# Optimization experiments

Measured on AMD Instinct MI355X. Metric: run time of the kernel, lower is better.

Reference implementation:

```python
import jax, jax.numpy as jnp
import numpy as np

N = 100000          # active voxels
KS = 7              # kernel size per spatial dim
K = KS ** 3         # 343 kernel offsets
G = 64              # voxel grid extent
INPLANES = 128
PLANES = 128
D2 = PLANES // 4    # 32
EPS = 1e-5


def _build_neighbor_map(seed=0):
    # Random distinct voxel coordinates in a G^3 grid, then for every point and
    # every 7^3 offset find the index of the neighboring voxel (-1 if absent).
    rng = np.random.default_rng(seed)
    lin = rng.choice(G ** 3, size=N, replace=False)
    coords = np.stack(np.unravel_index(lin, (G, G, G)), axis=1).astype(np.int64)  # [N,3]
    keys = coords[:, 0] * G * G + coords[:, 1] * G + coords[:, 2]
    order = np.argsort(keys)
    skeys = keys[order]
    offs = np.arange(KS) - KS // 2
    off_grid = np.stack(np.meshgrid(offs, offs, offs, indexing='ij'), axis=-1).reshape(K, 3)
    q = coords[:, None, :] + off_grid[None, :, :]          # [N,K,3]
    inb = np.all((q >= 0) & (q < G), axis=-1)
    qk = q[..., 0] * G * G + q[..., 1] * G + q[..., 2]
    pos = np.searchsorted(skeys, qk)
    pos_c = np.clip(pos, 0, N - 1)
    found = inb & (skeys[pos_c] == qk)
    nbr = np.where(found, order[pos_c], -1).astype(np.int32)  # [N,K]
    return jnp.asarray(nbr)


def setup_inputs() -> dict:
    key = jax.random.key(0)
    k = jax.random.split(key, 4)
    feats = jax.random.normal(k[0], (N, INPLANES), jnp.float32)
    w1 = jax.random.normal(k[1], (INPLANES, D2), jnp.float32) / np.sqrt(INPLANES)
    w_conv = jax.random.normal(k[2], (K, D2, D2), jnp.float32) / np.sqrt(K * D2)
    w2 = jax.random.normal(k[3], (D2, PLANES), jnp.float32) / np.sqrt(D2)
    return {
        'feats': feats,
        'nbr': _build_neighbor_map(),
        'w1': w1,
        'ln1_g': jnp.ones((D2,), jnp.float32),
        'ln1_b': jnp.zeros((D2,), jnp.float32),
        'w_conv': w_conv,
        'w2': w2,
        'ln2_g': jnp.ones((PLANES,), jnp.float32),
        'ln2_b': jnp.zeros((PLANES,), jnp.float32),
    }


def _layernorm(x, g, b):
    m = jnp.mean(x, axis=-1, keepdims=True)
    v = jnp.var(x, axis=-1, keepdims=True)
    return (x - m) * jax.lax.rsqrt(v + EPS) * g + b


def _sparse_conv(x, nbr, w):
    # x: [N,d2], nbr: [N,K], w: [K,d2,d2]; gather-apply-scatter per kernel offset.
    def step(acc, inp):
        idx, wk = inp                                # idx: [N], wk: [d2,d2]
        valid = (idx >= 0).astype(x.dtype)[:, None]
        g = jnp.take(x, jnp.maximum(idx, 0), axis=0) * valid
        return acc + g @ wk, None
    acc0 = jnp.zeros((x.shape[0], w.shape[2]), x.dtype)
    out, _ = jax.lax.scan(step, acc0, (nbr.T, w))
    return out


def reference(feats, nbr, w1, ln1_g, ln1_b, w_conv, w2, ln2_g, ln2_b):
    shortcut = feats                                  # inplanes == planes -> Identity
    h = _layernorm(feats @ w1, ln1_g, ln1_b)          # unary_1: [N,d2]
    h = _sparse_conv(h, nbr, w_conv)                  # 7^3 sparse conv: [N,d2]
    h = _layernorm(h @ w2, ln2_g, ln2_b)              # unary_2: [N,planes]
    h = jax.nn.gelu(h, approximate=False)             # drop_path is Identity (rate 0)
    return h + shortcut
```

## Files before the change

kernel.cpp:

```cpp
#include <hip/hip_runtime.h>
#include <hip/hip_bf16.h>

#define N_PTS 100000
#define KOFF 343
#define EPS 1e-5f
#define NTILES 3125
#define SSTR 173

typedef __hip_bfloat16 bf16;
typedef __attribute__((ext_vector_type(4))) float f32x4;
typedef __attribute__((ext_vector_type(16))) float f32x16;
typedef __attribute__((ext_vector_type(8))) short s16x8;

__global__ __launch_bounds__(256) void pack_kernel(const float* __restrict__ w_conv,
                                                   bf16* __restrict__ wpk) {
  int t = blockIdx.x * 256 + threadIdx.x;
  if (t >= KOFF * 128) return;
  int l = t & 63;
  int s = (t >> 6) & 1;
  int k = t >> 7;
  int col = l & 31;
  int kq = l >> 5;
  const float* wk = w_conv + k * 1024;
  s16x8 v;
  for (int j = 0; j < 8; ++j) {
    bf16 h = __float2bfloat16(wk[(s * 16 + kq * 8 + j) * 32 + col]);
    short sv;
    __builtin_memcpy(&sv, &h, 2);
    v[j] = sv;
  }
  *reinterpret_cast<s16x8*>(reinterpret_cast<char*>(wpk) + (size_t)t * 16) = v;
}

__global__ __launch_bounds__(256) void unary1_kernel(const float* __restrict__ feats,
    const float* __restrict__ w1, const float* __restrict__ g1,
    const float* __restrict__ b1, bf16* __restrict__ h1b) {
  __shared__ float sf[8][128];
  __shared__ float sw[128 * 32];
  int tid = threadIdx.x;
  int rbase = blockIdx.x * 8;
  for (int i = tid; i < 1024; i += 256)
    reinterpret_cast<f32x4*>(sw)[i] = reinterpret_cast<const f32x4*>(w1)[i];
  {
    int i = tid;
    int r = rbase + (i >> 5);
    f32x4 v = reinterpret_cast<const f32x4*>(feats)[(size_t)r * 32 + (i & 31)];
    reinterpret_cast<f32x4*>(&sf[0][0])[i] = v;
  }
  __syncthreads();
  int half = tid >> 5;
  int c = tid & 31;
  int r = rbase + half;
  const float* frow = sf[half];
  float acc = 0.f;
  #pragma unroll 8
  for (int kk = 0; kk < 128; ++kk)
    acc += frow[kk] * sw[kk * 32 + c];
  float s = acc, s2 = acc * acc;
  #pragma unroll
  for (int m = 16; m >= 1; m >>= 1) {
    s  += __shfl_xor(s,  m, 64);
    s2 += __shfl_xor(s2, m, 64);
  }
  float mean = s * (1.f / 32.f);
  float var  = s2 * (1.f / 32.f) - mean * mean;
  float y = (acc - mean) * rsqrtf(var + EPS) * g1[c] + b1[c];
  h1b[(size_t)r * 32 + c] = __float2bfloat16(y);
}

template<int KCNT, int KBASE>
__device__ __forceinline__ void process_round(const int* __restrict__ snbr,
    const bf16* __restrict__ h1b, const s16x8* __restrict__ wb,
    f32x16& acc, int wave, int l, int col, int kq) {
  int k0 = (KCNT * wave) >> 2;
  int k1 = (KCNT * (wave + 1)) >> 2;
  const int* myrow = snbr + col * SSTR;
  const s16x8 zv = {0, 0, 0, 0, 0, 0, 0, 0};
  for (int kb = k0; kb < k1; kb += 4) {
    int id[4];
    s16x8 A0[4], A1[4], B0[4], B1[4];
    #pragma unroll
    for (int j = 0; j < 4; ++j) {
      int k = kb + j;
      id[j] = (k < k1) ? myrow[k] : -1;
    }
    #pragma unroll
    for (int j = 0; j < 4; ++j) {
      int k = kb + j;
      int kc = (k < k1) ? k : (k1 - 1);
      const s16x8* r = reinterpret_cast<const s16x8*>(h1b + (size_t)(id[j] < 0 ? 0 : id[j]) * 32);
      A0[j] = r[kq];
      A1[j] = r[2 + kq];
      B0[j] = wb[(size_t)(KBASE + kc) * 128 + l];
      B1[j] = wb[(size_t)(KBASE + kc) * 128 + 64 + l];
    }
    #pragma unroll
    for (int j = 0; j < 4; ++j) {
      s16x8 a0 = id[j] < 0 ? zv : A0[j];
      s16x8 a1 = id[j] < 0 ? zv : A1[j];
      acc = __builtin_amdgcn_mfma_f32_32x32x16_bf16(a0, B0[j], acc, 0, 0, 0);
      acc = __builtin_amdgcn_mfma_f32_32x32x16_bf16(a1, B1[j], acc, 0, 0, 0);
    }
  }
}

__global__ __launch_bounds__(256) void conv_r2_kernel(const bf16* __restrict__ h1b,
    const int* __restrict__ nbr, const bf16* __restrict__ wpk,
    float* __restrict__ h2) {
  __shared__ int sbuf[32 * SSTR];
  int tid = threadIdx.x;
  int wave = tid >> 6;
  int l = tid & 63;
  int col = l & 31;
  int kq = l >> 5;
  int pbase = blockIdx.x * 32;
  const int* g = nbr + (size_t)pbase * KOFF;
  const s16x8* wb = reinterpret_cast<const s16x8*>(wpk);
  f32x16 acc;
  #pragma unroll
  for (int i = 0; i < 16; ++i) acc[i] = 0.f;

  for (int i = tid; i < 32 * 172; i += 256) {
    int row = i / 172;
    int kk = i - row * 172;
    sbuf[row * SSTR + kk] = g[row * KOFF + kk];
  }
  __syncthreads();
  process_round<172, 0>(sbuf, h1b, wb, acc, wave, l, col, kq);
  __syncthreads();
  for (int i = tid; i < 32 * 171; i += 256) {
    int row = i / 171;
    int kk = i - row * 171;
    sbuf[row * SSTR + kk] = g[row * KOFF + 172 + kk];
  }
  __syncthreads();
  process_round<171, 172>(sbuf, h1b, wb, acc, wave, l, col, kq);
  __syncthreads();

  float* red = reinterpret_cast<float*>(sbuf);
  #pragma unroll
  for (int reg = 0; reg < 16; ++reg) {
    int rrow = (reg & 3) + 8 * (reg >> 2) + 4 * kq;
    red[wave * 1024 + rrow * 32 + col] = acc[reg];
  }
  __syncthreads();
  const f32x4* rv = reinterpret_cast<const f32x4*>(red);
  f32x4 s = rv[tid] + rv[256 + tid] + rv[512 + tid] + rv[768 + tid];
  reinterpret_cast<f32x4*>(h2 + (size_t)pbase * 32)[tid] = s;
}

__global__ __launch_bounds__(256) void unary2_kernel(const float* __restrict__ h2,
    const float* __restrict__ w2, const float* __restrict__ g2,
    const float* __restrict__ b2, const float* __restrict__ feats,
    float* __restrict__ out) {
  int tid = threadIdx.x;
  int wave = tid >> 6;
  int l = tid & 63;
  int r0 = blockIdx.x * 8 + wave * 2;
  const f32x4* h0 = reinterpret_cast<const f32x4*>(h2 + (size_t)r0 * 32);
  const f32x4* h1r = reinterpret_cast<const f32x4*>(h2 + (size_t)(r0 + 1) * 32);
  float a00 = 0.f, a01 = 0.f, a10 = 0.f, a11 = 0.f;
  #pragma unroll
  for (int q = 0; q < 8; ++q) {
    f32x4 v0 = h0[q];
    f32x4 v1 = h1r[q];
    #pragma unroll
    for (int j = 0; j < 4; ++j) {
      int kk = q * 4 + j;
      float wlo = w2[kk * 128 + l];
      float whi = w2[kk * 128 + 64 + l];
      a00 += v0[j] * wlo;  a01 += v0[j] * whi;
      a10 += v1[j] * wlo;  a11 += v1[j] * whi;
    }
  }
  float s0 = a00 + a01, q0 = a00 * a00 + a01 * a01;
  float s1 = a10 + a11, q1 = a10 * a10 + a11 * a11;
  #pragma unroll
  for (int m = 32; m >= 1; m >>= 1) {
    s0 += __shfl_xor(s0, m, 64);
    q0 += __shfl_xor(q0, m, 64);
    s1 += __shfl_xor(s1, m, 64);
    q1 += __shfl_xor(q1, m, 64);
  }
  float m0 = s0 * (1.f / 128.f);
  float v0 = q0 * (1.f / 128.f) - m0 * m0;
  float i0 = rsqrtf(v0 + EPS);
  float m1 = s1 * (1.f / 128.f);
  float v1 = q1 * (1.f / 128.f) - m1 * m1;
  float i1 = rsqrtf(v1 + EPS);
  float glo = g2[l], ghi = g2[64 + l];
  float blo = b2[l], bhi = b2[64 + l];
  float y00 = (a00 - m0) * i0 * glo + blo;
  float y01 = (a01 - m0) * i0 * ghi + bhi;
  float y10 = (a10 - m1) * i1 * glo + blo;
  float y11 = (a11 - m1) * i1 * ghi + bhi;
  float e00 = 0.5f * y00 * (1.f + erff(y00 * 0.70710678118f));
  float e01 = 0.5f * y01 * (1.f + erff(y01 * 0.70710678118f));
  float e10 = 0.5f * y10 * (1.f + erff(y10 * 0.70710678118f));
  float e11 = 0.5f * y11 * (1.f + erff(y11 * 0.70710678118f));
  out[(size_t)r0 * 128 + l]            = e00 + feats[(size_t)r0 * 128 + l];
  out[(size_t)r0 * 128 + 64 + l]       = e01 + feats[(size_t)r0 * 128 + 64 + l];
  out[(size_t)(r0 + 1) * 128 + l]      = e10 + feats[(size_t)(r0 + 1) * 128 + l];
  out[(size_t)(r0 + 1) * 128 + 64 + l] = e11 + feats[(size_t)(r0 + 1) * 128 + 64 + l];
}

extern "C" void kernel_launch(void* const* d_in, const int* in_sizes, int n_in,
                              void* d_out, int out_size, void* d_ws, size_t ws_size,
                              hipStream_t stream) {
  const float* feats  = (const float*)d_in[0];
  const int*   nbr    = (const int*)d_in[1];
  const float* w1     = (const float*)d_in[2];
  const float* ln1_g  = (const float*)d_in[3];
  const float* ln1_b  = (const float*)d_in[4];
  const float* w_conv = (const float*)d_in[5];
  const float* w2     = (const float*)d_in[6];
  const float* ln2_g  = (const float*)d_in[7];
  const float* ln2_b  = (const float*)d_in[8];
  float* out = (float*)d_out;
  char* ws = (char*)d_ws;
  bf16*  h1b = (bf16*)ws;
  bf16*  wpk = (bf16*)(ws + 6400000);
  float* h2  = (float*)(ws + 7102464);

  hipLaunchKernelGGL(pack_kernel,    dim3((KOFF * 128 + 255) / 256), dim3(256), 0, stream, w_conv, wpk);
  hipLaunchKernelGGL(unary1_kernel,  dim3(N_PTS / 8),                dim3(256), 0, stream, feats, w1, ln1_g, ln1_b, h1b);
  hipLaunchKernelGGL(conv_r2_kernel, dim3(NTILES),                   dim3(256), 0, stream, h1b, nbr, wpk, h2);
  hipLaunchKernelGGL(unary2_kernel,  dim3(N_PTS / 8),                dim3(256), 0, stream, h2, w2, ln2_g, ln2_b, feats, out);
}
```

Measured before the change: 309.4 us.

## Switch sparse conv MFMA from 32x32x16 to four 16x16x32 tiles

Replaces the single 32x32x16 bf16 MFMA accumulator per wave with four 16x16x32 MFMAs covering two 16-point row groups and two 16-channel column halves. The packed weight layout and the gather pattern change to match, so each lane now loads a full 16-byte chunk of a neighbor row for two points. The aim is better gather coalescing, since more lanes share the same neighbor row, and use of the smaller MFMA shape. In exchange each wave issues twice as many MFMA instructions and more index loads from shared memory.

Result: slower. 316.0 us (+2.1%).

```diff
diff --git a/kernel.cpp b/kernel.cpp
--- a/kernel.cpp
+++ b/kernel.cpp
@@ -9,7 +9,6 @@
 
 typedef __hip_bfloat16 bf16;
 typedef __attribute__((ext_vector_type(4))) float f32x4;
-typedef __attribute__((ext_vector_type(16))) float f32x16;
 typedef __attribute__((ext_vector_type(8))) short s16x8;
 
 __global__ __launch_bounds__(256) void pack_kernel(const float* __restrict__ w_conv,
@@ -17,14 +16,14 @@
   int t = blockIdx.x * 256 + threadIdx.x;
   if (t >= KOFF * 128) return;
   int l = t & 63;
-  int s = (t >> 6) & 1;
+  int cn = (t >> 6) & 1;
   int k = t >> 7;
-  int col = l & 31;
-  int kq = l >> 5;
+  int rr = l & 15;
+  int q = l >> 4;
   const float* wk = w_conv + k * 1024;
   s16x8 v;
   for (int j = 0; j < 8; ++j) {
-    bf16 h = __float2bfloat16(wk[(s * 16 + kq * 8 + j) * 32 + col]);
+    bf16 h = __float2bfloat16(wk[(q * 8 + j) * 32 + cn * 16 + rr]);
     short sv;
     __builtin_memcpy(&sv, &h, 2);
     v[j] = sv;
@@ -71,54 +70,57 @@
 template<int KCNT, int KBASE>
 __device__ __forceinline__ void process_round(const int* __restrict__ snbr,
     const bf16* __restrict__ h1b, const s16x8* __restrict__ wb,
-    f32x16& acc, int wave, int l, int col, int kq) {
+    f32x4& acc00, f32x4& acc01, f32x4& acc10, f32x4& acc11, int wave, int l) {
   int k0 = (KCNT * wave) >> 2;
   int k1 = (KCNT * (wave + 1)) >> 2;
-  const int* myrow = snbr + col * SSTR;
+  int rr = l & 15;
+  int q = l >> 4;
+  const int* row0 = snbr + rr * SSTR;
+  const int* row1 = snbr + (16 + rr) * SSTR;
+  const s16x8* h1s8 = reinterpret_cast<const s16x8*>(h1b);
   const s16x8 zv = {0, 0, 0, 0, 0, 0, 0, 0};
   for (int kb = k0; kb < k1; kb += 4) {
-    int id[4];
+    int id0[4], id1[4];
     s16x8 A0[4], A1[4], B0[4], B1[4];
     #pragma unroll
     for (int j = 0; j < 4; ++j) {
       int k = kb + j;
-      id[j] = (k < k1) ? myrow[k] : -1;
+      id0[j] = (k < k1) ? row0[k] : -1;
+      id1[j] = (k < k1) ? row1[k] : -1;
     }
     #pragma unroll
     for (int j = 0; j < 4; ++j) {
       int k = kb + j;
       int kc = (k < k1) ? k : (k1 - 1);
-      const s16x8* r = reinterpret_cast<const s16x8*>(h1b + (size_t)(id[j] < 0 ? 0 : id[j]) * 32);
-      A0[j] = r[kq];
-      A1[j] = r[2 + kq];
+      A0[j] = h1s8[(size_t)(id0[j] < 0 ? 0 : id0[j]) * 4 + q];
+      A1[j] = h1s8[(size_t)(id1[j] < 0 ? 0 : id1[j]) * 4 + q];
       B0[j] = wb[(size_t)(KBASE + kc) * 128 + l];
       B1[j] = wb[(size_t)(KBASE + kc) * 128 + 64 + l];
     }
     #pragma unroll
     for (int j = 0; j < 4; ++j) {
-      s16x8 a0 = id[j] < 0 ? zv : A0[j];
-      s16x8 a1 = id[j] < 0 ? zv : A1[j];
-      acc = __builtin_amdgcn_mfma_f32_32x32x16_bf16(a0, B0[j], acc, 0, 0, 0);
-      acc = __builtin_amdgcn_mfma_f32_32x32x16_bf16(a1, B1[j], acc, 0, 0, 0);
-    }
-  }
-}
-
-__global__ __launch_bounds__(256) void conv_r2_kernel(const bf16* __restrict__ h1b,
+      s16x8 a0 = id0[j] < 0 ? zv : A0[j];
+      s16x8 a1 = id1[j] < 0 ? zv : A1[j];
+      acc00 = __builtin_amdgcn_mfma_f32_16x16x32_bf16(a0, B0[j], acc00, 0, 0, 0);
+      acc01 = __builtin_amdgcn_mfma_f32_16x16x32_bf16(a0, B1[j], acc01, 0, 0, 0);
+      acc10 = __builtin_amdgcn_mfma_f32_16x16x32_bf16(a1, B0[j], acc10, 0, 0, 0);
+      acc11 = __builtin_amdgcn_mfma_f32_16x16x32_bf16(a1, B1[j], acc11, 0, 0, 0);
+    }
+  }
+}
+
+__global__ __launch_bounds__(256) void conv16_kernel(const bf16* __restrict__ h1b,
     const int* __restrict__ nbr, const bf16* __restrict__ wpk,
     float* __restrict__ h2) {
   __shared__ int sbuf[32 * SSTR];
   int tid = threadIdx.x;
   int wave = tid >> 6;
   int l = tid & 63;
-  int col = l & 31;
-  int kq = l >> 5;
   int pbase = blockIdx.x * 32;
   const int* g = nbr + (size_t)pbase * KOFF;
   const s16x8* wb = reinterpret_cast<const s16x8*>(wpk);
-  f32x16 acc;
-  #pragma unroll
-  for (int i = 0; i < 16; ++i) acc[i] = 0.f;
+  f32x4 acc00 = {0.f, 0.f, 0.f, 0.f}, acc01 = {0.f, 0.f, 0.f, 0.f};
+  f32x4 acc10 = {0.f, 0.f, 0.f, 0.f}, acc11 = {0.f, 0.f, 0.f, 0.f};
 
   for (int i = tid; i < 32 * 172; i += 256) {
     int row = i / 172;
@@ -126,7 +128,7 @@
     sbuf[row * SSTR + kk] = g[row * KOFF + kk];
   }
   __syncthreads();
-  process_round<172, 0>(sbuf, h1b, wb, acc, wave, l, col, kq);
+  process_round<172, 0>(sbuf, h1b, wb, acc00, acc01, acc10, acc11, wave, l);
   __syncthreads();
   for (int i = tid; i < 32 * 171; i += 256) {
     int row = i / 171;
@@ -134,14 +136,19 @@
     sbuf[row * SSTR + kk] = g[row * KOFF + 172 + kk];
   }
   __syncthreads();
-  process_round<171, 172>(sbuf, h1b, wb, acc, wave, l, col, kq);
+  process_round<171, 172>(sbuf, h1b, wb, acc00, acc01, acc10, acc11, wave, l);
   __syncthreads();
 
   float* red = reinterpret_cast<float*>(sbuf);
-  #pragma unroll
-  for (int reg = 0; reg < 16; ++reg) {
-    int rrow = (reg & 3) + 8 * (reg >> 2) + 4 * kq;
-    red[wave * 1024 + rrow * 32 + col] = acc[reg];
+  int rr = l & 15;
+  int q = l >> 4;
+  #pragma unroll
+  for (int reg = 0; reg < 4; ++reg) {
+    int prow = q * 4 + reg;
+    red[wave * 1024 + prow * 32 + rr]             = acc00[reg];
+    red[wave * 1024 + prow * 32 + 16 + rr]        = acc01[reg];
+    red[wave * 1024 + (16 + prow) * 32 + rr]      = acc10[reg];
+    red[wave * 1024 + (16 + prow) * 32 + 16 + rr] = acc11[reg];
   }
   __syncthreads();
   const f32x4* rv = reinterpret_cast<const f32x4*>(red);
@@ -224,6 +231,6 @@
 
   hipLaunchKernelGGL(pack_kernel,    dim3((KOFF * 128 + 255) / 256), dim3(256), 0, stream, w_conv, wpk);
   hipLaunchKernelGGL(unary1_kernel,  dim3(N_PTS / 8),                dim3(256), 0, stream, feats, w1, ln1_g, ln1_b, h1b);
-  hipLaunchKernelGGL(conv_r2_kernel, dim3(NTILES),                   dim3(256), 0, stream, h1b, nbr, wpk, h2);
+  hipLaunchKernelGGL(conv16_kernel,  dim3(NTILES),                   dim3(256), 0, stream, h1b, nbr, wpk, h2);
   hipLaunchKernelGGL(unary2_kernel,  dim3(N_PTS / 8),                dim3(256), 0, stream, h2, w2, ln2_g, ln2_b, feats, out);
 }
```

## Restructure sparse conv so each wave owns 32 points and weights stage through LDS

Applied to the files above, without the earlier changes.

The conv kernel no longer splits the 343 offsets across four waves with a cross-wave LDS reduction. Each block now handles 128 points, one 32-point tile per wave, and walks all offsets in chunks of 16. Each chunk's neighbor indices and packed bf16 weights are staged into shared memory and reused by all four waves. Missing neighbors are redirected to an appended zero row of h1b, which removes the per-element select, and the weights are zero-padded to 352 offsets. The aim is to cut global weight traffic and the final reduction, at the cost of more barriers per block and fewer blocks (782 instead of 3125) for hiding gather latency.

Result: slower. 453.5 us (+46.6%).

```diff
diff --git a/kernel.cpp b/kernel.cpp
--- a/kernel.cpp
+++ b/kernel.cpp
@@ -3,9 +3,11 @@
 
 #define N_PTS 100000
 #define KOFF 343
+#define KPAD 352
+#define KC 16
+#define NCH 22
 #define EPS 1e-5f
-#define NTILES 3125
-#define SSTR 173
+#define SIDX_STR 17
 
 typedef __hip_bfloat16 bf16;
 typedef __attribute__((ext_vector_type(4))) float f32x4;
@@ -13,23 +15,25 @@
 typedef __attribute__((ext_vector_type(8))) short s16x8;
 
 __global__ __launch_bounds__(256) void pack_kernel(const float* __restrict__ w_conv,
-                                                   bf16* __restrict__ wpk) {
+                                                   bf16* __restrict__ wpk2) {
   int t = blockIdx.x * 256 + threadIdx.x;
-  if (t >= KOFF * 128) return;
+  if (t >= KPAD * 128) return;
   int l = t & 63;
   int s = (t >> 6) & 1;
   int k = t >> 7;
   int col = l & 31;
   int kq = l >> 5;
-  const float* wk = w_conv + k * 1024;
-  s16x8 v;
-  for (int j = 0; j < 8; ++j) {
-    bf16 h = __float2bfloat16(wk[(s * 16 + kq * 8 + j) * 32 + col]);
-    short sv;
-    __builtin_memcpy(&sv, &h, 2);
-    v[j] = sv;
-  }
-  *reinterpret_cast<s16x8*>(reinterpret_cast<char*>(wpk) + (size_t)t * 16) = v;
+  s16x8 v = {0, 0, 0, 0, 0, 0, 0, 0};
+  if (k < KOFF) {
+    const float* wk = w_conv + k * 1024;
+    for (int j = 0; j < 8; ++j) {
+      bf16 h = __float2bfloat16(wk[(s * 16 + kq * 8 + j) * 32 + col]);
+      short sv;
+      __builtin_memcpy(&sv, &h, 2);
+      v[j] = sv;
+    }
+  }
+  *reinterpret_cast<s16x8*>(reinterpret_cast<char*>(wpk2) + (size_t)t * 16) = v;
 }
 
 __global__ __launch_bounds__(256) void unary1_kernel(const float* __restrict__ feats,
@@ -39,6 +43,8 @@
   __shared__ float sw[128 * 32];
   int tid = threadIdx.x;
   int rbase = blockIdx.x * 8;
+  if (blockIdx.x == 0 && tid < 16)
+    reinterpret_cast<int*>(h1b)[N_PTS * 16 + tid] = 0;
   for (int i = tid; i < 1024; i += 256)
     reinterpret_cast<f32x4*>(sw)[i] = reinterpret_cast<const f32x4*>(w1)[i];
   {
@@ -68,85 +74,73 @@
   h1b[(size_t)r * 32 + c] = __float2bfloat16(y);
 }
 
-template<int KCNT, int KBASE>
-__device__ __forceinline__ void process_round(const int* __restrict__ snbr,
-    const bf16* __restrict__ h1b, const s16x8* __restrict__ wb,
-    f32x16& acc, int wave, int l, int col, int kq) {
-  int k0 = (KCNT * wave) >> 2;
-  int k1 = (KCNT * (wave + 1)) >> 2;
-  const int* myrow = snbr + col * SSTR;
-  const s16x8 zv = {0, 0, 0, 0, 0, 0, 0, 0};
-  for (int kb = k0; kb < k1; kb += 4) {
-    int id[4];
-    s16x8 A0[4], A1[4], B0[4], B1[4];
-    #pragma unroll
-    for (int j = 0; j < 4; ++j) {
-      int k = kb + j;
-      id[j] = (k < k1) ? myrow[k] : -1;
-    }
-    #pragma unroll
-    for (int j = 0; j < 4; ++j) {
-      int k = kb + j;
-      int kc = (k < k1) ? k : (k1 - 1);
-      const s16x8* r = reinterpret_cast<const s16x8*>(h1b + (size_t)(id[j] < 0 ? 0 : id[j]) * 32);
-      A0[j] = r[kq];
-      A1[j] = r[2 + kq];
-      B0[j] = wb[(size_t)(KBASE + kc) * 128 + l];
-      B1[j] = wb[(size_t)(KBASE + kc) * 128 + 64 + l];
-    }
-    #pragma unroll
-    for (int j = 0; j < 4; ++j) {
-      s16x8 a0 = id[j] < 0 ? zv : A0[j];
-      s16x8 a1 = id[j] < 0 ? zv : A1[j];
-      acc = __builtin_amdgcn_mfma_f32_32x32x16_bf16(a0, B0[j], acc, 0, 0, 0);
-      acc = __builtin_amdgcn_mfma_f32_32x32x16_bf16(a1, B1[j], acc, 0, 0, 0);
-    }
-  }
-}
-
-__global__ __launch_bounds__(256) void conv_r2_kernel(const bf16* __restrict__ h1b,
-    const int* __restrict__ nbr, const bf16* __restrict__ wpk,
+__global__ __launch_bounds__(256) void conv_ls_kernel(const bf16* __restrict__ h1b,
+    const int* __restrict__ nbr, const bf16* __restrict__ wpk2,
     float* __restrict__ h2) {
-  __shared__ int sbuf[32 * SSTR];
+  __shared__ int sidx[128 * SIDX_STR];
+  __shared__ s16x8 sB[KC * 128];
   int tid = threadIdx.x;
   int wave = tid >> 6;
   int l = tid & 63;
   int col = l & 31;
   int kq = l >> 5;
-  int pbase = blockIdx.x * 32;
-  const int* g = nbr + (size_t)pbase * KOFF;
-  const s16x8* wb = reinterpret_cast<const s16x8*>(wpk);
+  int pbase0 = blockIdx.x * 128;
+  const int* myrow = sidx + (wave * 32 + col) * SIDX_STR;
+  const s16x8* h1s = reinterpret_cast<const s16x8*>(h1b);
+  const s16x8* wsrc = reinterpret_cast<const s16x8*>(wpk2);
   f32x16 acc;
   #pragma unroll
   for (int i = 0; i < 16; ++i) acc[i] = 0.f;
 
-  for (int i = tid; i < 32 * 172; i += 256) {
-    int row = i / 172;
-    int kk = i - row * 172;
-    sbuf[row * SSTR + kk] = g[row * KOFF + kk];
-  }
-  __syncthreads();
-  process_round<172, 0>(sbuf, h1b, wb, acc, wave, l, col, kq);
-  __syncthreads();
-  for (int i = tid; i < 32 * 171; i += 256) {
-    int row = i / 171;
-    int kk = i - row * 171;
-    sbuf[row * SSTR + kk] = g[row * KOFF + 172 + kk];
-  }
-  __syncthreads();
-  process_round<171, 172>(sbuf, h1b, wb, acc, wave, l, col, kq);
-  __syncthreads();
-
-  float* red = reinterpret_cast<float*>(sbuf);
+  for (int ch = 0; ch < NCH; ++ch) {
+    int kbase = ch * KC;
+    #pragma unroll
+    for (int i = 0; i < 8; ++i) {
+      int e = i * 256 + tid;
+      int p = e >> 4;
+      int kk = e & 15;
+      int pg = pbase0 + p;
+      int k = kbase + kk;
+      int v = (pg < N_PTS && k < KOFF) ? nbr[(size_t)pg * KOFF + k] : -1;
+      sidx[p * SIDX_STR + kk] = v < 0 ? N_PTS : v;
+    }
+    {
+      const s16x8* src = wsrc + (size_t)kbase * 128;
+      #pragma unroll
+      for (int i = 0; i < 8; ++i)
+        sB[i * 256 + tid] = src[i * 256 + tid];
+    }
+    __syncthreads();
+    #pragma unroll
+    for (int kb = 0; kb < KC; kb += 4) {
+      int id[4];
+      #pragma unroll
+      for (int j = 0; j < 4; ++j) id[j] = myrow[kb + j];
+      s16x8 A0[4], A1[4], B0[4], B1[4];
+      #pragma unroll
+      for (int j = 0; j < 4; ++j) {
+        const s16x8* r = h1s + (size_t)id[j] * 4;
+        A0[j] = r[kq];
+        A1[j] = r[2 + kq];
+        B0[j] = sB[(kb + j) * 128 + l];
+        B1[j] = sB[(kb + j) * 128 + 64 + l];
+      }
+      #pragma unroll
+      for (int j = 0; j < 4; ++j) {
+        acc = __builtin_amdgcn_mfma_f32_32x32x16_bf16(A0[j], B0[j], acc, 0, 0, 0);
+        acc = __builtin_amdgcn_mfma_f32_32x32x16_bf16(A1[j], B1[j], acc, 0, 0, 0);
+      }
+    }
+    __syncthreads();
+  }
+
+  int pb = pbase0 + wave * 32;
   #pragma unroll
   for (int reg = 0; reg < 16; ++reg) {
     int rrow = (reg & 3) + 8 * (reg >> 2) + 4 * kq;
-    red[wave * 1024 + rrow * 32 + col] = acc[reg];
-  }
-  __syncthreads();
-  const f32x4* rv = reinterpret_cast<const f32x4*>(red);
-  f32x4 s = rv[tid] + rv[256 + tid] + rv[512 + tid] + rv[768 + tid];
-  reinterpret_cast<f32x4*>(h2 + (size_t)pbase * 32)[tid] = s;
+    int row = pb + rrow;
+    if (row < N_PTS) h2[(size_t)row * 32 + col] = acc[reg];
+  }
 }
 
 __global__ __launch_bounds__(256) void unary2_kernel(const float* __restrict__ h2,
@@ -218,12 +212,12 @@
   const float* ln2_b  = (const float*)d_in[8];
   float* out = (float*)d_out;
   char* ws = (char*)d_ws;
-  bf16*  h1b = (bf16*)ws;
-  bf16*  wpk = (bf16*)(ws + 6400000);
-  float* h2  = (float*)(ws + 7102464);
-
-  hipLaunchKernelGGL(pack_kernel,    dim3((KOFF * 128 + 255) / 256), dim3(256), 0, stream, w_conv, wpk);
+  bf16*  h1b  = (bf16*)ws;
+  bf16*  wpk2 = (bf16*)(ws + 6400064);
+  float* h2   = (float*)(ws + 7120960);
+
+  hipLaunchKernelGGL(pack_kernel,    dim3((KPAD * 128 + 255) / 256), dim3(256), 0, stream, w_conv, wpk2);
   hipLaunchKernelGGL(unary1_kernel,  dim3(N_PTS / 8),                dim3(256), 0, stream, feats, w1, ln1_g, ln1_b, h1b);
-  hipLaunchKernelGGL(conv_r2_kernel, dim3(NTILES),                   dim3(256), 0, stream, h1b, nbr, wpk, h2);
+  hipLaunchKernelGGL(conv_ls_kernel, dim3((N_PTS + 127) / 128),      dim3(256), 0, stream, h1b, nbr, wpk2, h2);
   hipLaunchKernelGGL(unary2_kernel,  dim3(N_PTS / 8),                dim3(256), 0, stream, h2, w2, ln2_g, ln2_b, feats, out);
 }
```

## Give each wave its own 32 points with all offsets, drop cross-wave reduction

Applied to the files above, without the earlier changes.

The conv kernel now gives each of the four waves its own 32-point tile and has it walk all 343 offsets, instead of splitting the offsets of one tile across waves. This removes the shared-memory cross-wave reduction and its final sync. Missing neighbours now point at a zeroed dummy row appended to h1b, so the per-lane select on the gathered data goes away. Neighbour ids are prefetched one step ahead. Each wave now reads every weight slice itself, which raises weight-load traffic per point, and blocks become larger with fewer of them.

Result: slower. 408.7 us (+32.1%).

```diff
diff --git a/kernel.cpp b/kernel.cpp
--- a/kernel.cpp
+++ b/kernel.cpp
@@ -4,8 +4,7 @@
 #define N_PTS 100000
 #define KOFF 343
 #define EPS 1e-5f
-#define NTILES 3125
-#define SSTR 173
+#define SSTR 87
 
 typedef __hip_bfloat16 bf16;
 typedef __attribute__((ext_vector_type(4))) float f32x4;
@@ -39,6 +38,8 @@
   __shared__ float sw[128 * 32];
   int tid = threadIdx.x;
   int rbase = blockIdx.x * 8;
+  if (blockIdx.x == 0 && tid < 16)
+    reinterpret_cast<int*>(h1b)[N_PTS * 16 + tid] = 0;
   for (int i = tid; i < 1024; i += 256)
     reinterpret_cast<f32x4*>(sw)[i] = reinterpret_cast<const f32x4*>(w1)[i];
   {
@@ -69,84 +70,88 @@
 }
 
 template<int KCNT, int KBASE>
-__device__ __forceinline__ void process_round(const int* __restrict__ snbr,
+__device__ __forceinline__ void stage_round(const int* __restrict__ nbr,
+    int* __restrict__ sbuf, int tid, int pbase0) {
+  for (int i = tid; i < 128 * KCNT; i += 256) {
+    int row = i / KCNT;
+    int kk = i - row * KCNT;
+    int p = pbase0 + row;
+    int v = (p < N_PTS) ? nbr[(size_t)p * KOFF + KBASE + kk] : -1;
+    sbuf[row * SSTR + kk] = v < 0 ? N_PTS : v;
+  }
+}
+
+template<int KCNT, int KBASE>
+__device__ __forceinline__ void process_round(const int* __restrict__ sbuf,
     const bf16* __restrict__ h1b, const s16x8* __restrict__ wb,
     f32x16& acc, int wave, int l, int col, int kq) {
-  int k0 = (KCNT * wave) >> 2;
-  int k1 = (KCNT * (wave + 1)) >> 2;
-  const int* myrow = snbr + col * SSTR;
-  const s16x8 zv = {0, 0, 0, 0, 0, 0, 0, 0};
-  for (int kb = k0; kb < k1; kb += 4) {
-    int id[4];
+  const int* myrow = sbuf + (wave * 32 + col) * SSTR;
+  const s16x8* h1s = reinterpret_cast<const s16x8*>(h1b);
+  int id[4];
+  #pragma unroll
+  for (int j = 0; j < 4; ++j) id[j] = (j < KCNT) ? myrow[j] : N_PTS;
+  for (int kb = 0; kb < KCNT; kb += 4) {
     s16x8 A0[4], A1[4], B0[4], B1[4];
     #pragma unroll
     for (int j = 0; j < 4; ++j) {
-      int k = kb + j;
-      id[j] = (k < k1) ? myrow[k] : -1;
-    }
-    #pragma unroll
-    for (int j = 0; j < 4; ++j) {
-      int k = kb + j;
-      int kc = (k < k1) ? k : (k1 - 1);
-      const s16x8* r = reinterpret_cast<const s16x8*>(h1b + (size_t)(id[j] < 0 ? 0 : id[j]) * 32);
+      const s16x8* r = h1s + (size_t)id[j] * 4;
       A0[j] = r[kq];
       A1[j] = r[2 + kq];
+      int kc = (kb + j < KCNT) ? kb + j : KCNT - 1;
       B0[j] = wb[(size_t)(KBASE + kc) * 128 + l];
       B1[j] = wb[(size_t)(KBASE + kc) * 128 + 64 + l];
     }
+    int idn[4];
+    #pragma unroll
+    for (int j = 0; j < 4; ++j) idn[j] = (kb + 4 + j < KCNT) ? myrow[kb + 4 + j] : N_PTS;
     #pragma unroll
     for (int j = 0; j < 4; ++j) {
-      s16x8 a0 = id[j] < 0 ? zv : A0[j];
-      s16x8 a1 = id[j] < 0 ? zv : A1[j];
-      acc = __builtin_amdgcn_mfma_f32_32x32x16_bf16(a0, B0[j], acc, 0, 0, 0);
-      acc = __builtin_amdgcn_mfma_f32_32x32x16_bf16(a1, B1[j], acc, 0, 0, 0);
+      acc = __builtin_amdgcn_mfma_f32_32x32x16_bf16(A0[j], B0[j], acc, 0, 0, 0);
+      acc = __builtin_amdgcn_mfma_f32_32x32x16_bf16(A1[j], B1[j], acc, 0, 0, 0);
     }
-  }
-}
-
-__global__ __launch_bounds__(256) void conv_r2_kernel(const bf16* __restrict__ h1b,
+    #pragma unroll
+    for (int j = 0; j < 4; ++j) id[j] = idn[j];
+  }
+}
+
+__global__ __launch_bounds__(256) void conv_lk_kernel(const bf16* __restrict__ h1b,
     const int* __restrict__ nbr, const bf16* __restrict__ wpk,
     float* __restrict__ h2) {
-  __shared__ int sbuf[32 * SSTR];
+  __shared__ int sbuf[128 * SSTR];
   int tid = threadIdx.x;
   int wave = tid >> 6;
   int l = tid & 63;
   int col = l & 31;
   int kq = l >> 5;
-  int pbase = blockIdx.x * 32;
-  const int* g = nbr + (size_t)pbase * KOFF;
+  int pbase0 = blockIdx.x * 128;
   const s16x8* wb = reinterpret_cast<const s16x8*>(wpk);
   f32x16 acc;
   #pragma unroll
   for (int i = 0; i < 16; ++i) acc[i] = 0.f;
 
-  for (int i = tid; i < 32 * 172; i += 256) {
-    int row = i / 172;
-    int kk = i - row * 172;
-    sbuf[row * SSTR + kk] = g[row * KOFF + kk];
-  }
-  __syncthreads();
-  process_round<172, 0>(sbuf, h1b, wb, acc, wave, l, col, kq);
-  __syncthreads();
-  for (int i = tid; i < 32 * 171; i += 256) {
-    int row = i / 171;
-    int kk = i - row * 171;
-    sbuf[row * SSTR + kk] = g[row * KOFF + 172 + kk];
-  }
-  __syncthreads();
-  process_round<171, 172>(sbuf, h1b, wb, acc, wave, l, col, kq);
-  __syncthreads();
-
-  float* red = reinterpret_cast<float*>(sbuf);
+  stage_round<86, 0>(nbr, sbuf, tid, pbase0);
+  __syncthreads();
+  process_round<86, 0>(sbuf, h1b, wb, acc, wave, l, col, kq);
+  __syncthreads();
+  stage_round<86, 86>(nbr, sbuf, tid, pbase0);
+  __syncthreads();
+  process_round<86, 86>(sbuf, h1b, wb, acc, wave, l, col, kq);
+  __syncthreads();
+  stage_round<86, 172>(nbr, sbuf, tid, pbase0);
+  __syncthreads();
+  process_round<86, 172>(sbuf, h1b, wb, acc, wave, l, col, kq);
+  __syncthreads();
+  stage_round<85, 258>(nbr, sbuf, tid, pbase0);
+  __syncthreads();
+  process_round<85, 258>(sbuf, h1b, wb, acc, wave, l, col, kq);
+
+  int pb = pbase0 + wave * 32;
   #pragma unroll
   for (int reg = 0; reg < 16; ++reg) {
     int rrow = (reg & 3) + 8 * (reg >> 2) + 4 * kq;
-    red[wave * 1024 + rrow * 32 + col] = acc[reg];
-  }
-  __syncthreads();
-  const f32x4* rv = reinterpret_cast<const f32x4*>(red);
-  f32x4 s = rv[tid] + rv[256 + tid] + rv[512 + tid] + rv[768 + tid];
-  reinterpret_cast<f32x4*>(h2 + (size_t)pbase * 32)[tid] = s;
+    int row = pb + rrow;
+    if (row < N_PTS) h2[(size_t)row * 32 + col] = acc[reg];
+  }
 }
 
 __global__ __launch_bounds__(256) void unary2_kernel(const float* __restrict__ h2,
@@ -219,11 +224,11 @@
   float* out = (float*)d_out;
   char* ws = (char*)d_ws;
   bf16*  h1b = (bf16*)ws;
-  bf16*  wpk = (bf16*)(ws + 6400000);
-  float* h2  = (float*)(ws + 7102464);
+  bf16*  wpk = (bf16*)(ws + 6400064);
+  float* h2  = (float*)(ws + 7102528);
 
   hipLaunchKernelGGL(pack_kernel,    dim3((KOFF * 128 + 255) / 256), dim3(256), 0, stream, w_conv, wpk);
   hipLaunchKernelGGL(unary1_kernel,  dim3(N_PTS / 8),                dim3(256), 0, stream, feats, w1, ln1_g, ln1_b, h1b);
-  hipLaunchKernelGGL(conv_r2_kernel, dim3(NTILES),                   dim3(256), 0, stream, h1b, nbr, wpk, h2);
+  hipLaunchKernelGGL(conv_lk_kernel, dim3((N_PTS + 127) / 128),      dim3(256), 0, stream, h1b, nbr, wpk, h2);
   hipLaunchKernelGGL(unary2_kernel,  dim3(N_PTS / 8),                dim3(256), 0, stream, h2, w2, ln2_g, ln2_b, feats, out);
 }
```
